# Kernel optimization log

Measured on AMD Instinct MI355X. Metric: run time of the kernel, lower is better.

Reference implementation:

```python
import jax, jax.numpy as jnp
import numpy as np

N = 50000   # nodes
E = 800000  # edges
R = 8       # relations
IN, HID, OUT = 512, 256, 512


def _rgcn_conv(x, W, root, b, src, dst, etype):
    """PyG RGCNConv with aggr='mean': out[i] = x[i]@root + b + sum_r mean_{j->i, rel=r} x[j]@W_r.
    Uses aggregate-then-transform (valid by linearity) to avoid [E, in, out] tensors."""
    n = x.shape[0]
    seg = etype * n + dst                                   # per-(relation, dst) segment id
    cnt = jax.ops.segment_sum(jnp.ones((E,), x.dtype), seg, num_segments=R * n)
    inv = jnp.where(cnt > 0, 1.0 / cnt, 0.0)                # mean normalization per (rel, dst)
    msg = x[src] * inv[seg][:, None]                        # [E, in]
    agg = jax.ops.segment_sum(msg, seg, num_segments=R * n) # [R*n, in]
    agg = agg.reshape(R, n, -1)
    return jnp.einsum('rni,rio->no', agg, W) + x @ root + b


def _l2_normalize(x, eps=1e-12):
    return x / jnp.maximum(jnp.linalg.norm(x, axis=-1, keepdims=True), eps)


def setup_inputs() -> dict:
    key = jax.random.key(0)
    ks = jax.random.split(key, 10)
    s = lambda fan_in: 1.0 / np.sqrt(fan_in)
    return {
        'x': jax.random.normal(ks[0], (N, IN), jnp.float32),
        'W1': jax.random.normal(ks[1], (R, IN, HID), jnp.float32) * s(IN),
        'root1': jax.random.normal(ks[2], (IN, HID), jnp.float32) * s(IN),
        'b1': jax.random.normal(ks[3], (HID,), jnp.float32) * 0.01,
        'W2': jax.random.normal(ks[4], (R, HID, OUT), jnp.float32) * s(HID),
        'root2': jax.random.normal(ks[5], (HID, OUT), jnp.float32) * s(HID),
        'b2': jax.random.normal(ks[6], (OUT,), jnp.float32) * 0.01,
        'src': jax.random.randint(ks[7], (E,), 0, N, jnp.int32),
        'dst': jax.random.randint(ks[8], (E,), 0, N, jnp.int32),
        'edge_type': jax.random.randint(ks[9], (E,), 0, R, jnp.int32),
    }


def reference(x, W1, root1, b1, W2, root2, b2, src, dst, edge_type):
    h = _rgcn_conv(x, W1, root1, b1, src, dst, edge_type)
    h = jax.nn.relu(h)
    h = _rgcn_conv(h, W2, root2, b2, src, dst, edge_type)
    return _l2_normalize(h)  # dropout is identity in eval mode
```

## Files before the change

kernel.cpp:

```cpp
#include <hip/hip_runtime.h>
#include <hip/hip_bf16.h>
#include <stdint.h>

#define NN   50000
#define EE   800000
#define RR   8
#define CIN  512
#define CHID 256
#define COUT 512
#define SEGS (RR * NN)
#define MHALF 25000
#define K2   2304
#define K2S  2048

typedef _Float16 f16;
typedef _Float16 f16x8 __attribute__((ext_vector_type(8)));
typedef _Float16 f16x4 __attribute__((ext_vector_type(4)));
typedef float    f32x4 __attribute__((ext_vector_type(4)));

constexpr int SCAN_BS = 256, SCAN_ITEMS = 4, SCAN_CHUNK = SCAN_BS * SCAN_ITEMS;
constexpr int SCAN_NB = (SEGS + SCAN_CHUNK - 1) / SCAN_CHUNK;

__device__ __forceinline__ f32x4 mfma_f16(f16x8 a, f16x8 b, f32x4 c) {
    return __builtin_amdgcn_mfma_f32_16x16x32_f16(a, b, c, 0, 0, 0);
}

__device__ __forceinline__ void gload_lds16(const void* g, void* l) {
    __builtin_amdgcn_global_load_lds((const __attribute__((address_space(1))) void*)g,
                                     (__attribute__((address_space(3))) void*)l, 16, 0, 0);
}

__global__ void cvt16(const float* __restrict__ in, f16* __restrict__ o, int n8) {
    int i = blockIdx.x * blockDim.x + threadIdx.x;
    if (i >= n8) return;
    f32x4 a = ((const f32x4*)in)[2 * i];
    f32x4 b = ((const f32x4*)in)[2 * i + 1];
    f16x8 v;
#pragma unroll
    for (int j = 0; j < 4; ++j) { v[j] = (f16)a[j]; v[4 + j] = (f16)b[j]; }
    ((f16x8*)o)[i] = v;
}

__global__ void wprep16(const float* __restrict__ W, f16* __restrict__ o,
                        int K0, int NC, int Ktot, int koffbase, int koffstride,
                        int relstride) {
    int r = blockIdx.z;
    int idx = blockIdx.x * blockDim.x + threadIdx.x;
    if (idx >= K0 * NC) return;
    int k = idx / NC, c = idx % NC;
    float v = W[(size_t)r * K0 * NC + idx];
    o[(size_t)r * relstride + (size_t)c * Ktot + koffbase + r * koffstride + k] = (f16)v;
}

__global__ void count_edges(const int* __restrict__ et, const int* __restrict__ dst,
                            int* __restrict__ cnt) {
    int e = blockIdx.x * blockDim.x + threadIdx.x;
    if (e < EE) atomicAdd(&cnt[et[e] * NN + dst[e]], 1);
}

__global__ void scan_partial(const int* __restrict__ cnt, int* __restrict__ bsum) {
    __shared__ int lds[SCAN_BS];
    const int b = blockIdx.x, t = threadIdx.x;
    const int base = b * SCAN_CHUNK + t * SCAN_ITEMS;
    int s = 0;
#pragma unroll
    for (int j = 0; j < SCAN_ITEMS; ++j) {
        int i = base + j;
        if (i < SEGS) s += cnt[i];
    }
    lds[t] = s;
    __syncthreads();
    for (int off = SCAN_BS / 2; off > 0; off >>= 1) {
        if (t < off) lds[t] += lds[t + off];
        __syncthreads();
    }
    if (t == 0) bsum[b] = lds[0];
}

__global__ void scan_bsum(int* __restrict__ bsum) {
    __shared__ int lds[512];
    const int t = threadIdx.x;
    const int v = (t < SCAN_NB) ? bsum[t] : 0;
    lds[t] = v;
    __syncthreads();
    for (int off = 1; off < 512; off <<= 1) {
        int x = (t >= off) ? lds[t - off] : 0;
        __syncthreads();
        lds[t] += x;
        __syncthreads();
    }
    if (t < SCAN_NB) bsum[t] = lds[t] - v;
}

__global__ void scan_final(const int* __restrict__ cnt, const int* __restrict__ bsum,
                           int* __restrict__ cursor) {
    __shared__ int lds[SCAN_BS];
    const int b = blockIdx.x, t = threadIdx.x;
    const int base = b * SCAN_CHUNK + t * SCAN_ITEMS;
    int v[SCAN_ITEMS];
    int s = 0;
#pragma unroll
    for (int j = 0; j < SCAN_ITEMS; ++j) {
        int i = base + j;
        v[j] = (i < SEGS) ? cnt[i] : 0;
        s += v[j];
    }
    lds[t] = s;
    __syncthreads();
    for (int off = 1; off < SCAN_BS; off <<= 1) {
        int x = (t >= off) ? lds[t - off] : 0;
        __syncthreads();
        lds[t] += x;
        __syncthreads();
    }
    int run = lds[t] - s + bsum[b];
#pragma unroll
    for (int j = 0; j < SCAN_ITEMS; ++j) {
        int i = base + j;
        if (i < SEGS) cursor[i] = run;
        run += v[j];
    }
}

__global__ void bucket_fill(const int* __restrict__ src, const int* __restrict__ dst,
                            const int* __restrict__ et, int* __restrict__ cursor,
                            int* __restrict__ esrc) {
    int e = blockIdx.x * blockDim.x + threadIdx.x;
    if (e < EE) {
        int s = et[e] * NN + dst[e];
        int pos = atomicAdd(&cursor[s], 1);
        esrc[pos] = src[e];
    }
}

template <int K, int K1, int SA1, int SA2, int NC, int EPI>
__global__ __launch_bounds__(256, 4) void gemm16(
    const f16* __restrict__ A1, const f16* __restrict__ A2,
    const f16* __restrict__ B, float* __restrict__ C,
    const float* __restrict__ bias, f16* __restrict__ O16, int M) {
    __shared__ f16 lds[16384];
    f16* sA = lds;
    f16* sB = lds + 8192;
    constexpr int NT = NC / 128;

    const int nwg = gridDim.x;
    const int orig = blockIdx.x;
    const int q8 = nwg >> 3, r8 = nwg & 7;
    const int xcd = orig & 7, lin = orig >> 3;
    const int wg = (xcd < r8 ? xcd * (q8 + 1) : r8 * (q8 + 1) + (xcd - r8) * q8) + lin;
    const int mtile = wg / NT, ntile = wg % NT;
    const int row0 = mtile * 128, col0 = ntile * 128;

    const int t = threadIdx.x;
    const int lane = t & 63;
    const int wid = t >> 6;
    const int wm = wid >> 1, wn = wid & 1;
    const int fr = lane & 15;

    f32x4 acc[4][4] = {};

    for (int ks = 0; ks < K / 64; ++ks) {
        const int k0 = ks * 64;
        const bool useA2 = (K1 < K) && (k0 >= K1);
        const f16* Ab = useA2 ? A2 : A1;
        const int astr = useA2 ? SA2 : SA1;
        const int ak0 = useA2 ? k0 - K1 : k0;
#pragma unroll
        for (int i = 0; i < 4; ++i) {
            const int flat = i * 256 + t;
            const int rr = flat >> 3;
            const int scol = ((flat & 7) ^ (rr & 7)) * 8;
            int ra = row0 + rr;
            ra = ra < M ? ra : M - 1;
            gload_lds16(Ab + (size_t)ra * astr + ak0 + scol, sA + flat * 8);
            gload_lds16(B + (size_t)(col0 + rr) * K + k0 + scol, sB + flat * 8);
        }
        __syncthreads();
#pragma unroll
        for (int kk = 0; kk < 2; ++kk) {
            const int ch = ((kk * 4 + (lane >> 4)) ^ (fr & 7)) * 8;
            f16x8 fa[4], fb[4];
#pragma unroll
            for (int m = 0; m < 4; ++m)
                fa[m] = *(const f16x8*)(sA + (wm * 64 + m * 16 + fr) * 64 + ch);
#pragma unroll
            for (int n = 0; n < 4; ++n)
                fb[n] = *(const f16x8*)(sB + (wn * 64 + n * 16 + fr) * 64 + ch);
#pragma unroll
            for (int m = 0; m < 4; ++m)
#pragma unroll
                for (int n = 0; n < 4; ++n)
                    acc[m][n] = mfma_f16(fa[m], fb[n], acc[m][n]);
        }
        __syncthreads();
    }

#pragma unroll
    for (int m = 0; m < 4; ++m)
#pragma unroll
        for (int n = 0; n < 4; ++n)
#pragma unroll
            for (int qq = 0; qq < 4; ++qq) {
                int row = row0 + wm * 64 + m * 16 + (lane >> 4) * 4 + qq;
                int col = col0 + wn * 64 + n * 16 + fr;
                if (row < M) {
                    size_t o = (size_t)row * NC + col;
                    float v = acc[m][n][qq];
                    if (EPI == 0) O16[o] = (f16)v;
                    else C[o] = v + bias[col];
                }
            }
}

__global__ void gather_l1_pair(const f16* __restrict__ xW0, const f16* __restrict__ xW1,
                               const int* __restrict__ esrc, const int* __restrict__ cursor,
                               const int* __restrict__ cnt, float* __restrict__ h_pre,
                               int rel0) {
    const int d = blockIdx.x * 4 + (threadIdx.x >> 6);
    if (d >= NN) return;
    const int lane = threadIdx.x & 63;
    const int s0 = rel0 * NN + d;
    const int s1 = s0 + NN;
    const int n0 = cnt[s0], n1 = cnt[s1];
    if ((n0 | n1) == 0) return;
    f32x4 v = {};
    if (n0 > 0) {
        const int end = cursor[s0];
        f32x4 acc = {};
        for (int i = end - n0; i < end; ++i) {
            f16x4 a = *(const f16x4*)(xW0 + (size_t)esrc[i] * CHID + lane * 4);
#pragma unroll
            for (int j = 0; j < 4; ++j) acc[j] += (float)a[j];
        }
        v += acc * (1.0f / (float)n0);
    }
    if (n1 > 0) {
        const int end = cursor[s1];
        f32x4 acc = {};
        for (int i = end - n1; i < end; ++i) {
            f16x4 a = *(const f16x4*)(xW1 + (size_t)esrc[i] * CHID + lane * 4);
#pragma unroll
            for (int j = 0; j < 4; ++j) acc[j] += (float)a[j];
        }
        v += acc * (1.0f / (float)n1);
    }
    ((f32x4*)(h_pre + (size_t)d * CHID))[lane] += v;
}

__global__ void finish1(const float* __restrict__ h_pre, f16* __restrict__ hh) {
    int i = blockIdx.x * blockDim.x + threadIdx.x;
    if (i >= NN * CHID / 4) return;
    f32x4 v = ((const f32x4*)h_pre)[i];
    f16x4 a;
#pragma unroll
    for (int j = 0; j < 4; ++j) a[j] = (f16)fmaxf(v[j], 0.0f);
    ((f16x4*)hh)[i] = a;
}

__global__ void gather_g2(const f16* __restrict__ hh, const int* __restrict__ esrc,
                          const int* __restrict__ cursor, const int* __restrict__ cnt,
                          f16* __restrict__ G2h, int half) {
    const int sidx = blockIdx.x * 4 + (threadIdx.x >> 6);
    if (sidx >= RR * MHALF) return;
    const int lane = threadIdx.x & 63;
    const int rel = sidx / MHALF;
    const int dloc = sidx % MHALF;
    const int d = half * MHALF + dloc;
    const int s = rel * NN + d;
    const int n = cnt[s];
    f32x4 v = {};
    if (n > 0) {
        const int end = cursor[s];
        for (int i = end - n; i < end; ++i) {
            f16x4 a = *(const f16x4*)(hh + (size_t)esrc[i] * CHID + lane * 4);
#pragma unroll
            for (int j = 0; j < 4; ++j) v[j] += (float)a[j];
        }
        const float inv = 1.0f / (float)n;
#pragma unroll
        for (int j = 0; j < 4; ++j) v[j] *= inv;
    }
    f16x4 o;
#pragma unroll
    for (int j = 0; j < 4; ++j) o[j] = (f16)v[j];
    *(f16x4*)(G2h + (size_t)dloc * K2S + rel * CHID + lane * 4) = o;
}

__global__ void l2norm(float* __restrict__ out) {
    int row = blockIdx.x * 4 + (threadIdx.x >> 6);
    int lane = threadIdx.x & 63;
    if (row >= NN) return;
    float* p = out + (size_t)row * COUT;
    f32x4 a = ((const f32x4*)p)[lane];
    f32x4 b = ((const f32x4*)p)[lane + 64];
    float ss = a[0] * a[0] + a[1] * a[1] + a[2] * a[2] + a[3] * a[3] +
               b[0] * b[0] + b[1] * b[1] + b[2] * b[2] + b[3] * b[3];
#pragma unroll
    for (int m = 32; m >= 1; m >>= 1) ss += __shfl_xor(ss, m, 64);
    const float s = 1.0f / fmaxf(sqrtf(ss), 1e-12f);
#pragma unroll
    for (int j = 0; j < 4; ++j) { a[j] *= s; b[j] *= s; }
    ((f32x4*)p)[lane] = a;
    ((f32x4*)p)[lane + 64] = b;
}

extern "C" void kernel_launch(void* const* d_in, const int* in_sizes, int n_in,
                              void* d_out, int out_size, void* d_ws, size_t ws_size,
                              hipStream_t stream) {
    (void)in_sizes; (void)n_in; (void)out_size; (void)ws_size;
    const float* x  = (const float*)d_in[0];
    const float* W1 = (const float*)d_in[1];
    const float* r1 = (const float*)d_in[2];
    const float* b1 = (const float*)d_in[3];
    const float* W2 = (const float*)d_in[4];
    const float* r2 = (const float*)d_in[5];
    const float* b2 = (const float*)d_in[6];
    const int* src = (const int*)d_in[7];
    const int* dst = (const int*)d_in[8];
    const int* et  = (const int*)d_in[9];
    float* out = (float*)d_out;

    char* w = (char*)d_ws;
    auto take = [&](size_t bytes) {
        char* p = w;
        w += (bytes + 255) & ~(size_t)255;
        return p;
    };
    int* cnt    = (int*)take((size_t)SEGS * 4);
    int* cursor = (int*)take((size_t)SEGS * 4);
    int* bsum   = (int*)take((size_t)SCAN_NB * 4);
    int* esrc   = (int*)take((size_t)EE * 4);
    f16* x16  = (f16*)take((size_t)NN * CIN * 2);
    f16* hh   = (f16*)take((size_t)NN * CHID * 2);
    f16* W1t  = (f16*)take((size_t)RR * CIN * CHID * 2);
    f16* r1t  = (f16*)take((size_t)CIN * CHID * 2);
    f16* W2c  = (f16*)take((size_t)COUT * K2 * 2);
    char* arena = take((size_t)MHALF * K2S * 2);
    f16*   xW0   = (f16*)arena;
    f16*   xW1   = (f16*)(arena + (size_t)NN * CHID * 2);
    float* h_pre = (float*)(arena + (size_t)NN * CHID * 4);
    f16*   G2h   = (f16*)arena;

    hipMemsetAsync(cnt, 0, (size_t)SEGS * 4, stream);

    cvt16<<<(NN * CIN / 8 + 255) / 256, 256, 0, stream>>>(x, x16, NN * CIN / 8);
    wprep16<<<dim3((CIN * CHID + 255) / 256, 1, RR), 256, 0, stream>>>(
        W1, W1t, CIN, CHID, CIN, 0, 0, CIN * CHID);
    wprep16<<<dim3((CIN * CHID + 255) / 256, 1, 1), 256, 0, stream>>>(
        r1, r1t, CIN, CHID, CIN, 0, 0, 0);
    wprep16<<<dim3((CHID * COUT + 255) / 256, 1, RR), 256, 0, stream>>>(
        W2, W2c, CHID, COUT, K2, 0, CHID, 0);
    wprep16<<<dim3((CHID * COUT + 255) / 256, 1, 1), 256, 0, stream>>>(
        r2, W2c, CHID, COUT, K2, K2S, 0, 0);

    count_edges<<<(EE + 255) / 256, 256, 0, stream>>>(et, dst, cnt);
    scan_partial<<<SCAN_NB, SCAN_BS, 0, stream>>>(cnt, bsum);
    scan_bsum<<<1, 512, 0, stream>>>(bsum);
    scan_final<<<SCAN_NB, SCAN_BS, 0, stream>>>(cnt, bsum, cursor);
    bucket_fill<<<(EE + 255) / 256, 256, 0, stream>>>(src, dst, et, cursor, esrc);

    const int MT1 = (NN + 127) / 128;
    const int MT2 = (MHALF + 127) / 128;

    gemm16<CIN, CIN, CIN, CIN, CHID, 3><<<MT1 * 2, 256, 0, stream>>>(
        x16, x16, r1t, h_pre, b1, nullptr, NN);
    for (int rp = 0; rp < RR / 2; ++rp) {
        const int rel = rp * 2;
        gemm16<CIN, CIN, CIN, CIN, CHID, 0><<<MT1 * 2, 256, 0, stream>>>(
            x16, x16, W1t + (size_t)rel * CIN * CHID, nullptr, nullptr, xW0, NN);
        gemm16<CIN, CIN, CIN, CIN, CHID, 0><<<MT1 * 2, 256, 0, stream>>>(
            x16, x16, W1t + (size_t)(rel + 1) * CIN * CHID, nullptr, nullptr, xW1, NN);
        gather_l1_pair<<<(NN + 3) / 4, 256, 0, stream>>>(xW0, xW1, esrc, cursor, cnt,
                                                         h_pre, rel);
    }
    finish1<<<(NN * CHID / 4 + 255) / 256, 256, 0, stream>>>(h_pre, hh);

    for (int half = 0; half < 2; ++half) {
        gather_g2<<<(RR * MHALF + 3) / 4, 256, 0, stream>>>(hh, esrc, cursor, cnt,
                                                            G2h, half);
        gemm16<K2, K2S, K2S, CHID, COUT, 3><<<MT2 * 4, 256, 0, stream>>>(
            G2h, hh + (size_t)half * MHALF * CHID, W2c,
            out + (size_t)half * MHALF * COUT, b2, nullptr, MHALF);
    }

    l2norm<<<(NN + 3) / 4, 256, 0, stream>>>(out);
}
```

Baseline: 1.024 ms.

## Merge layer-1 relation GEMMs into one wide GEMM and fuse gather with ReLU

```diff
diff --git a/kernel.cpp b/kernel.cpp
--- a/kernel.cpp
+++ b/kernel.cpp
@@ -9,9 +9,9 @@
 #define CHID 256
 #define COUT 512
 #define SEGS (RR * NN)
-#define MHALF 25000
 #define K2   2304
 #define K2S  2048
+#define N1   2304
 
 typedef _Float16 f16;
 typedef _Float16 f16x8 __attribute__((ext_vector_type(8)));
@@ -204,73 +204,56 @@
                 int row = row0 + wm * 64 + m * 16 + (lane >> 4) * 4 + qq;
                 int col = col0 + wn * 64 + n * 16 + fr;
                 if (row < M) {
-                    size_t o = (size_t)row * NC + col;
                     float v = acc[m][n][qq];
-                    if (EPI == 0) O16[o] = (f16)v;
-                    else C[o] = v + bias[col];
+                    if (EPI == 3) {
+                        C[(size_t)row * NC + col] = v + bias[col];
+                    } else {
+                        if (col < K2S) O16[(size_t)row * K2S + col] = (f16)v;
+                        else C[(size_t)row * CHID + (col - K2S)] = v + bias[col - K2S];
+                    }
                 }
             }
 }
 
-__global__ void gather_l1_pair(const f16* __restrict__ xW0, const f16* __restrict__ xW1,
-                               const int* __restrict__ esrc, const int* __restrict__ cursor,
-                               const int* __restrict__ cnt, float* __restrict__ h_pre,
-                               int rel0) {
+__global__ void gather_l1(const f16* __restrict__ xWall, const int* __restrict__ esrc,
+                          const int* __restrict__ cursor, const int* __restrict__ cnt,
+                          const float* __restrict__ h_pre, f16* __restrict__ hh) {
     const int d = blockIdx.x * 4 + (threadIdx.x >> 6);
     if (d >= NN) return;
     const int lane = threadIdx.x & 63;
-    const int s0 = rel0 * NN + d;
-    const int s1 = s0 + NN;
-    const int n0 = cnt[s0], n1 = cnt[s1];
-    if ((n0 | n1) == 0) return;
-    f32x4 v = {};
-    if (n0 > 0) {
-        const int end = cursor[s0];
+    f32x4 v = ((const f32x4*)(h_pre + (size_t)d * CHID))[lane];
+#pragma unroll
+    for (int rel = 0; rel < RR; ++rel) {
+        const int s = rel * NN + d;
+        const int n = cnt[s];
+        if (n == 0) continue;
+        const int end = cursor[s];
         f32x4 acc = {};
-        for (int i = end - n0; i < end; ++i) {
-            f16x4 a = *(const f16x4*)(xW0 + (size_t)esrc[i] * CHID + lane * 4);
+        for (int i = end - n; i < end; ++i) {
+            f16x4 a = *(const f16x4*)(xWall + (size_t)esrc[i] * K2S + rel * CHID + lane * 4);
 #pragma unroll
             for (int j = 0; j < 4; ++j) acc[j] += (float)a[j];
         }
-        v += acc * (1.0f / (float)n0);
-    }
-    if (n1 > 0) {
-        const int end = cursor[s1];
-        f32x4 acc = {};
-        for (int i = end - n1; i < end; ++i) {
-            f16x4 a = *(const f16x4*)(xW1 + (size_t)esrc[i] * CHID + lane * 4);
-#pragma unroll
-            for (int j = 0; j < 4; ++j) acc[j] += (float)a[j];
-        }
-        v += acc * (1.0f / (float)n1);
-    }
-    ((f32x4*)(h_pre + (size_t)d * CHID))[lane] += v;
-}
-
-__global__ void finish1(const float* __restrict__ h_pre, f16* __restrict__ hh) {
-    int i = blockIdx.x * blockDim.x + threadIdx.x;
-    if (i >= NN * CHID / 4) return;
-    f32x4 v = ((const f32x4*)h_pre)[i];
-    f16x4 a;
-#pragma unroll
-    for (int j = 0; j < 4; ++j) a[j] = (f16)fmaxf(v[j], 0.0f);
-    ((f16x4*)hh)[i] = a;
+        v += acc * (1.0f / (float)n);
+    }
+    f16x4 o;
+#pragma unroll
+    for (int j = 0; j < 4; ++j) o[j] = (f16)fmaxf(v[j], 0.0f);
+    *(f16x4*)(hh + (size_t)d * CHID + lane * 4) = o;
 }
 
 __global__ void gather_g2(const f16* __restrict__ hh, const int* __restrict__ esrc,
                           const int* __restrict__ cursor, const int* __restrict__ cnt,
-                          f16* __restrict__ G2h, int half) {
+                          f16* __restrict__ G2) {
     const int sidx = blockIdx.x * 4 + (threadIdx.x >> 6);
-    if (sidx >= RR * MHALF) return;
+    if (sidx >= SEGS) return;
     const int lane = threadIdx.x & 63;
-    const int rel = sidx / MHALF;
-    const int dloc = sidx % MHALF;
-    const int d = half * MHALF + dloc;
-    const int s = rel * NN + d;
-    const int n = cnt[s];
+    const int rel = sidx / NN;
+    const int d = sidx % NN;
+    const int n = cnt[sidx];
     f32x4 v = {};
     if (n > 0) {
-        const int end = cursor[s];
+        const int end = cursor[sidx];
         for (int i = end - n; i < end; ++i) {
             f16x4 a = *(const f16x4*)(hh + (size_t)esrc[i] * CHID + lane * 4);
 #pragma unroll
@@ -283,7 +266,7 @@
     f16x4 o;
 #pragma unroll
     for (int j = 0; j < 4; ++j) o[j] = (f16)v[j];
-    *(f16x4*)(G2h + (size_t)dloc * K2S + rel * CHID + lane * 4) = o;
+    *(f16x4*)(G2 + (size_t)d * K2S + rel * CHID + lane * 4) = o;
 }
 
 __global__ void l2norm(float* __restrict__ out) {
@@ -330,24 +313,22 @@
     int* cursor = (int*)take((size_t)SEGS * 4);
     int* bsum   = (int*)take((size_t)SCAN_NB * 4);
     int* esrc   = (int*)take((size_t)EE * 4);
-    f16* x16  = (f16*)take((size_t)NN * CIN * 2);
-    f16* hh   = (f16*)take((size_t)NN * CHID * 2);
-    f16* W1t  = (f16*)take((size_t)RR * CIN * CHID * 2);
-    f16* r1t  = (f16*)take((size_t)CIN * CHID * 2);
-    f16* W2c  = (f16*)take((size_t)COUT * K2 * 2);
-    char* arena = take((size_t)MHALF * K2S * 2);
-    f16*   xW0   = (f16*)arena;
-    f16*   xW1   = (f16*)(arena + (size_t)NN * CHID * 2);
-    float* h_pre = (float*)(arena + (size_t)NN * CHID * 4);
-    f16*   G2h   = (f16*)arena;
+    f16*   x16   = (f16*)take((size_t)NN * CIN * 2);
+    f16*   hh    = (f16*)take((size_t)NN * CHID * 2);
+    float* h_pre = (float*)take((size_t)NN * CHID * 4);
+    f16*   W1c   = (f16*)take((size_t)N1 * CIN * 2);
+    f16*   W2c   = (f16*)take((size_t)COUT * K2 * 2);
+    char* arena = take((size_t)NN * K2S * 2);
+    f16* xWall = (f16*)arena;
+    f16* G2    = (f16*)arena;
 
     hipMemsetAsync(cnt, 0, (size_t)SEGS * 4, stream);
 
     cvt16<<<(NN * CIN / 8 + 255) / 256, 256, 0, stream>>>(x, x16, NN * CIN / 8);
     wprep16<<<dim3((CIN * CHID + 255) / 256, 1, RR), 256, 0, stream>>>(
-        W1, W1t, CIN, CHID, CIN, 0, 0, CIN * CHID);
+        W1, W1c, CIN, CHID, CIN, 0, 0, CHID * CIN);
     wprep16<<<dim3((CIN * CHID + 255) / 256, 1, 1), 256, 0, stream>>>(
-        r1, r1t, CIN, CHID, CIN, 0, 0, 0);
+        r1, W1c, CIN, CHID, CIN, K2S * CIN, 0, 0);
     wprep16<<<dim3((CHID * COUT + 255) / 256, 1, RR), 256, 0, stream>>>(
         W2, W2c, CHID, COUT, K2, 0, CHID, 0);
     wprep16<<<dim3((CHID * COUT + 255) / 256, 1, 1), 256, 0, stream>>>(
@@ -359,29 +340,15 @@
     scan_final<<<SCAN_NB, SCAN_BS, 0, stream>>>(cnt, bsum, cursor);
     bucket_fill<<<(EE + 255) / 256, 256, 0, stream>>>(src, dst, et, cursor, esrc);
 
-    const int MT1 = (NN + 127) / 128;
-    const int MT2 = (MHALF + 127) / 128;
-
-    gemm16<CIN, CIN, CIN, CIN, CHID, 3><<<MT1 * 2, 256, 0, stream>>>(
-        x16, x16, r1t, h_pre, b1, nullptr, NN);
-    for (int rp = 0; rp < RR / 2; ++rp) {
-        const int rel = rp * 2;
-        gemm16<CIN, CIN, CIN, CIN, CHID, 0><<<MT1 * 2, 256, 0, stream>>>(
-            x16, x16, W1t + (size_t)rel * CIN * CHID, nullptr, nullptr, xW0, NN);
-        gemm16<CIN, CIN, CIN, CIN, CHID, 0><<<MT1 * 2, 256, 0, stream>>>(
-            x16, x16, W1t + (size_t)(rel + 1) * CIN * CHID, nullptr, nullptr, xW1, NN);
-        gather_l1_pair<<<(NN + 3) / 4, 256, 0, stream>>>(xW0, xW1, esrc, cursor, cnt,
-                                                         h_pre, rel);
-    }
-    finish1<<<(NN * CHID / 4 + 255) / 256, 256, 0, stream>>>(h_pre, hh);
-
-    for (int half = 0; half < 2; ++half) {
-        gather_g2<<<(RR * MHALF + 3) / 4, 256, 0, stream>>>(hh, esrc, cursor, cnt,
-                                                            G2h, half);
-        gemm16<K2, K2S, K2S, CHID, COUT, 3><<<MT2 * 4, 256, 0, stream>>>(
-            G2h, hh + (size_t)half * MHALF * CHID, W2c,
-            out + (size_t)half * MHALF * COUT, b2, nullptr, MHALF);
-    }
+    const int MT = (NN + 127) / 128;
+
+    gemm16<CIN, CIN, CIN, CIN, N1, 4><<<MT * (N1 / 128), 256, 0, stream>>>(
+        x16, x16, W1c, h_pre, b1, xWall, NN);
+    gather_l1<<<(NN + 3) / 4, 256, 0, stream>>>(xWall, esrc, cursor, cnt, h_pre, hh);
+
+    gather_g2<<<(SEGS + 3) / 4, 256, 0, stream>>>(hh, esrc, cursor, cnt, G2);
+    gemm16<K2, K2S, K2S, CHID, COUT, 3><<<MT * (COUT / 128), 256, 0, stream>>>(
+        G2, hh, W2c, out, b2, nullptr, NN);
 
     l2norm<<<(NN + 3) / 4, 256, 0, stream>>>(out);
 }
```

New measurement: 971.4 us. 5.2% less time.
